# Kernel tuning notes

Measured on AMD Instinct MI355X. Metric: run time of the kernel, lower is better.

Reference implementation:

```python
import jax, jax.numpy as jnp
import numpy as np

B, CHAR_LEN, LSTM, VOCAB, NATTN = 4096, 64, 400, 73, 10

def _lstm_cell(x, h, c, W_ih, W_hh, b):
    # gates: [B, 4*LSTM] in (i, f, g, o) order, matching torch.nn.LSTMCell
    g = x @ W_ih.T + h @ W_hh.T + b
    i, f, gg, o = jnp.split(g, 4, axis=1)
    i = jax.nn.sigmoid(i); f = jax.nn.sigmoid(f)
    gg = jnp.tanh(gg); o = jax.nn.sigmoid(o)
    c_new = f * c + i * gg
    h_new = o * jnp.tanh(c_new)
    return h_new, c_new

def setup_inputs() -> dict:
    key = jax.random.key(0)
    ks = jax.random.split(key, 24)
    d = {}
    d['inputs'] = jax.random.normal(ks[0], (B, 3), jnp.float32)
    for n, k in zip(['h1','c1','h2','c2','h3','c3'], ks[1:7]):
        d[n] = jax.random.normal(k, (B, LSTM), jnp.float32) * 0.1
    d['kappa'] = jax.random.uniform(ks[7], (B, NATTN), jnp.float32) * 5.0
    d['w_prev'] = jax.random.uniform(ks[8], (B, VOCAB), jnp.float32)
    d['attention_values'] = jax.random.uniform(ks[9], (B, CHAR_LEN, VOCAB), jnp.float32)
    d['attention_lengths'] = jax.random.randint(ks[10], (B,), 1, CHAR_LEN + 1, jnp.int32)
    s = 0.05
    in1 = VOCAB + 3              # lstm1 input: [w, inputs]
    in23 = 3 + LSTM + VOCAB      # lstm2/3 input: [inputs, h, w]
    attn_in = VOCAB + 3 + LSTM
    d['W_ih1'] = jax.random.normal(ks[11], (4 * LSTM, in1), jnp.float32) * s
    d['W_hh1'] = jax.random.normal(ks[12], (4 * LSTM, LSTM), jnp.float32) * s
    d['b1'] = jax.random.normal(ks[13], (4 * LSTM,), jnp.float32) * s
    d['W_attn'] = jax.random.normal(ks[14], (3 * NATTN, attn_in), jnp.float32) * s
    d['b_attn'] = jax.random.normal(ks[15], (3 * NATTN,), jnp.float32) * s
    d['W_ih2'] = jax.random.normal(ks[16], (4 * LSTM, in23), jnp.float32) * s
    d['W_hh2'] = jax.random.normal(ks[17], (4 * LSTM, LSTM), jnp.float32) * s
    d['b2'] = jax.random.normal(ks[18], (4 * LSTM,), jnp.float32) * s
    d['W_ih3'] = jax.random.normal(ks[19], (4 * LSTM, in23), jnp.float32) * s
    d['W_hh3'] = jax.random.normal(ks[20], (4 * LSTM, LSTM), jnp.float32) * s
    d['b3'] = jax.random.normal(ks[21], (4 * LSTM,), jnp.float32) * s
    return d

def reference(inputs, h1, c1, h2, c2, h3, c3, kappa, w_prev, attention_values,
              attention_lengths, W_ih1, W_hh1, b1, W_attn, b_attn,
              W_ih2, W_hh2, b2, W_ih3, W_hh3, b3):
    char_len = attention_values.shape[1]
    # --- LSTM 1 ---
    s1_in = jnp.concatenate([w_prev, inputs], axis=1)
    h1n, c1n = _lstm_cell(s1_in, h1, c1, W_ih1, W_hh1, b1)
    # --- Gaussian-mixture location attention ---
    attn_in = jnp.concatenate([w_prev, inputs, h1n], axis=1)
    attn_params = jax.nn.softplus(attn_in @ W_attn.T + b_attn)
    alpha, beta, kap = jnp.split(attn_params, 3, axis=1)
    kap = kappa + kap / 25.0
    beta = jnp.maximum(beta, 0.01)
    u = jnp.arange(char_len, dtype=jnp.float32)[None, None, :]           # [1,1,C]
    phi = jnp.sum(alpha[:, :, None] *
                  jnp.exp(-jnp.square(kap[:, :, None] - u) / beta[:, :, None]),
                  axis=1)                                                 # [B,C]
    seq_mask = (jnp.arange(char_len)[None, :] < attention_lengths[:, None]).astype(jnp.float32)
    w = jnp.einsum('bc,bcv->bv', phi * seq_mask, attention_values)        # [B,V]
    # --- LSTM 2 & 3 ---
    s2_in = jnp.concatenate([inputs, h1n, w], axis=1)
    h2n, c2n = _lstm_cell(s2_in, h2, c2, W_ih2, W_hh2, b2)
    s3_in = jnp.concatenate([inputs, h2n, w], axis=1)
    h3n, c3n = _lstm_cell(s3_in, h3, c3, W_ih3, W_hh3, b3)
    return h3n
```

## Files before the change

kernel.cpp:

```cpp
#include <hip/hip_runtime.h>
#include <hip/hip_bf16.h>


#define B_SZ     4096
#define LSTM_N   400
#define NG       1600
#define VOCAB    73
#define NATTN    10
#define CHARLEN  64
#define KP1      512
#define KP23     896

typedef _Float16 half8 __attribute__((ext_vector_type(8)));
typedef __attribute__((ext_vector_type(4))) float floatx4;

__device__ __forceinline__ void gload_lds16(const void* g, void* l) {
    __builtin_amdgcn_global_load_lds(
        (const __attribute__((address_space(1))) void*)g,
        (__attribute__((address_space(3))) void*)l, 16, 0, 0);
}

__device__ __forceinline__ int lds_off(int r, int g) {
    return (r << 6) + ((((g ^ r) & 7)) << 3);
}

#define CW1   102400
#define CW23  179200
#define CWA   4096
#define CX1   262144
#define CXA   57344
#define CX23  253952
#define O1    (CW1)
#define O2    (O1 + CW23)
#define O3    (O2 + CW23)
#define O4    (O3 + CWA)
#define O5    (O4 + CX1)
#define O6    (O5 + CXA)
#define O7    (O6 + CX23)

__global__ __launch_bounds__(256) void pack_all(const float* __restrict__ Wih1,
                                                const float* __restrict__ Whh1,
                                                const float* __restrict__ Wih2,
                                                const float* __restrict__ Whh2,
                                                const float* __restrict__ Wih3,
                                                const float* __restrict__ Whh3,
                                                const float* __restrict__ W_attn,
                                                const float* __restrict__ w_prev,
                                                const float* __restrict__ inputs,
                                                const float* __restrict__ h1,
                                                const float* __restrict__ h2,
                                                const float* __restrict__ h3,
                                                _Float16* __restrict__ W1,
                                                _Float16* __restrict__ W2,
                                                _Float16* __restrict__ W3,
                                                _Float16* __restrict__ Wa,
                                                _Float16* __restrict__ X1,
                                                _Float16* __restrict__ XA,
                                                _Float16* __restrict__ X2,
                                                _Float16* __restrict__ X3)
{
    const int id = blockIdx.x * 256 + threadIdx.x;
    half8 hv;

    if (id < O1) {
        const int row = id >> 6;
        const int k0  = (id & 63) << 3;
        const int u = row >> 2, g = row & 3;
        const int src = g * 400 + u;
#pragma unroll
        for (int e = 0; e < 8; e++) {
            const int k = k0 + e;
            float x = 0.f;
            if (k < 76)           x = Wih1[(size_t)src * 76 + k];
            else if (k < 476)     x = Whh1[(size_t)src * 400 + (k - 76)];
            hv[e] = (_Float16)x;
        }
        *(half8*)(W1 + (size_t)row * KP1 + k0) = hv;
    } else if (id < O3) {
        const int id2 = id - O1;
        const bool is3 = (id2 >= CW23);
        const int id3 = is3 ? id2 - CW23 : id2;
        const int row = id3 / 112;
        const int k0  = (id3 - row * 112) << 3;
        const int u = row >> 2, g = row & 3;
        const int src = g * 400 + u;
        const float* Wih = is3 ? Wih3 : Wih2;
        const float* Whh = is3 ? Whh3 : Whh2;
#pragma unroll
        for (int e = 0; e < 8; e++) {
            const int k = k0 + e;
            float x = 0.f;
            if (k < 400)          x = Wih[(size_t)src * 476 + 3 + k];
            else if (k < 403)     x = Wih[(size_t)src * 476 + (k - 400)];
            else if (k < 476)     x = Wih[(size_t)src * 476 + k];
            else if (k < 876)     x = Whh[(size_t)src * 400 + (k - 476)];
            hv[e] = (_Float16)x;
        }
        *(half8*)((is3 ? W3 : W2) + (size_t)row * KP23 + k0) = hv;
    } else if (id < O4) {
        const int id4 = id - O3;
        const int row = id4 >> 6;
        const int k0  = (id4 & 63) << 3;
#pragma unroll
        for (int e = 0; e < 8; e++) {
            const int k = k0 + e;
            float x = 0.f;
            if (row < 30) {
                if (k < 400)      x = W_attn[(size_t)row * 476 + 76 + k];
                else if (k < 473) x = W_attn[(size_t)row * 476 + (k - 400)];
                else if (k < 476) x = W_attn[(size_t)row * 476 + 73 + (k - 473)];
            }
            hv[e] = (_Float16)x;
        }
        *(half8*)(Wa + (size_t)row * KP1 + k0) = hv;
    } else if (id < O5) {
        const int id5 = id - O4;
        const int b  = id5 >> 6;
        const int k0 = (id5 & 63) << 3;
#pragma unroll
        for (int e = 0; e < 8; e++) {
            const int k = k0 + e;
            float x = 0.f;
            if (k < 73)           x = w_prev[(size_t)b * 73 + k];
            else if (k < 76)      x = inputs[(size_t)b * 3 + (k - 73)];
            else if (k < 476)     x = h1[(size_t)b * 400 + (k - 76)];
            hv[e] = (_Float16)x;
        }
        *(half8*)(X1 + (size_t)b * KP1 + k0) = hv;
    } else if (id < O6) {
        const int id6 = id - O5;
        const int b  = id6 / 14;
        const int k0 = 400 + ((id6 - b * 14) << 3);
#pragma unroll
        for (int e = 0; e < 8; e++) {
            const int k = k0 + e;
            float x = 0.f;
            if (k < 473)          x = w_prev[(size_t)b * 73 + (k - 400)];
            else if (k < 476)     x = inputs[(size_t)b * 3 + (k - 473)];
            hv[e] = (_Float16)x;
        }
        *(half8*)(XA + (size_t)b * KP1 + k0) = hv;
    } else if (id < O7) {
        const int id7 = id - O6;
        const int b  = id7 / 62;
        const int k0 = 400 + ((id7 - b * 62) << 3);
        half8 h2v, h3v;
#pragma unroll
        for (int e = 0; e < 8; e++) {
            const int k = k0 + e;
            float x2 = 0.f, x3 = 0.f;
            if (k < 403)                    { x2 = inputs[(size_t)b * 3 + (k - 400)]; x3 = x2; }
            else if (k >= 476 && k < 876)   { x2 = h2[(size_t)b * 400 + (k - 476)];
                                              x3 = h3[(size_t)b * 400 + (k - 476)]; }
            h2v[e] = (_Float16)x2;
            h3v[e] = (_Float16)x3;
        }
        *(half8*)(X2 + (size_t)b * KP23 + k0) = h2v;
        *(half8*)(X3 + (size_t)b * KP23 + k0) = h3v;
    }
}

template<int KP>
__global__ __launch_bounds__(256) void gemm_fused_t(const _Float16* __restrict__ Wm,
                                                    const _Float16* __restrict__ X,
                                                    const float* __restrict__ bias,
                                                    const float* __restrict__ c_in,
                                                    _Float16* __restrict__ d1, int ld1,
                                                    _Float16* __restrict__ d2, int ld2,
                                                    float* __restrict__ fout)
{
    __shared__ _Float16 lds[3][192 * 64];

    const int t    = threadIdx.x;
    const int w    = t >> 6;
    const int lane = t & 63;
    const int quad = lane >> 4;
    const int l16  = lane & 15;
    const int fid  = blockIdx.y * 32 + blockIdx.x;
    const int xcd  = fid & 7;
    const int loc  = fid >> 3;
    const int bx   = xcd * 4 + loc / 25;
    const int by   = loc % 25;
    const int m0   = by * 64;
    const int n0   = bx * 128;
    const int wm   = (w >> 1) * 32;
    const int wn   = (w & 1) * 64;
    const int lr   = lane >> 3;
    const int gq   = (lane & 7) ^ lr;

    floatx4 acc[2][4] = {};

    auto stage = [&](int sb, int k0) {
#pragma unroll
        for (int s = 0; s < 2; s++)
            gload_lds16(Wm + (size_t)(m0 + w * 16 + s * 8 + lr) * KP + k0 + gq * 8,
                        &lds[sb][(w * 16 + s * 8) * 64]);
#pragma unroll
        for (int s = 0; s < 4; s++)
            gload_lds16(X + (size_t)(n0 + w * 32 + s * 8 + lr) * KP + k0 + gq * 8,
                        &lds[sb][(64 + w * 32 + s * 8) * 64]);
    };

    stage(0, 0);
    stage(1, 64);
    constexpr int NT = KP / 64;
#pragma unroll
    for (int kt = 0; kt < NT; kt++) {
        const int sb = kt % 3;
        if (kt + 2 < NT) {
            stage((kt + 2) % 3, (kt + 2) * 64);
            asm volatile("s_waitcnt vmcnt(12)" ::: "memory");
        } else if (kt + 1 < NT) {
            asm volatile("s_waitcnt vmcnt(6)" ::: "memory");
        } else {
            asm volatile("s_waitcnt vmcnt(0)" ::: "memory");
        }
        __builtin_amdgcn_s_barrier();
        __builtin_amdgcn_sched_barrier(0);

#pragma unroll
        for (int h = 0; h < 2; h++) {
            half8 af[2], bf[4];
#pragma unroll
            for (int i = 0; i < 2; i++)
                af[i] = *(const half8*)(&lds[sb][lds_off(wm + i * 16 + l16, h * 4 + quad)]);
#pragma unroll
            for (int i = 0; i < 4; i++)
                bf[i] = *(const half8*)(&lds[sb][lds_off(64 + wn + i * 16 + l16, h * 4 + quad)]);
            __builtin_amdgcn_s_setprio(1);
#pragma unroll
            for (int mt = 0; mt < 2; mt++)
#pragma unroll
                for (int nt = 0; nt < 4; nt++)
                    acc[mt][nt] = __builtin_amdgcn_mfma_f32_16x16x32_f16(
                        af[mt], bf[nt], acc[mt][nt], 0, 0, 0);
            __builtin_amdgcn_s_setprio(0);
        }
        __builtin_amdgcn_s_barrier();
    }
    __builtin_amdgcn_sched_barrier(0);

    const int u0 = m0 >> 2;
    float*    Cs   = (float*)&lds[0][0];
    _Float16* Hs16 = (_Float16*)&lds[1][0];
    float*    Hs32 = (float*)&lds[1][0];
    {
        const int bl = t >> 1;
        const int j0 = (t & 1) * 2;
#pragma unroll
        for (int j = 0; j < 2; j++) {
            floatx4 cv = *(const floatx4*)(c_in + (size_t)(n0 + bl) * LSTM_N
                                           + u0 + (j0 + j) * 4);
            *(floatx4*)(Cs + bl * 20 + (j0 + j) * 4) = cv;
        }
    }
    __syncthreads();

#pragma unroll
    for (int mt = 0; mt < 2; mt++) {
        const int ul = (wm >> 2) + mt * 4 + quad;
        const int u  = u0 + ul;
        const float bi  = bias[u];
        const float bff = bias[400 + u];
        const float bg  = bias[800 + u];
        const float bo  = bias[1200 + u];
#pragma unroll
        for (int nt = 0; nt < 4; nt++) {
            const int bl = wn + nt * 16 + l16;
            float gi = acc[mt][nt][0] + bi;
            float gf = acc[mt][nt][1] + bff;
            float gg = acc[mt][nt][2] + bg;
            float go = acc[mt][nt][3] + bo;
            float si = 1.f / (1.f + expf(-gi));
            float sf = 1.f / (1.f + expf(-gf));
            float so = 1.f / (1.f + expf(-go));
            float cn = sf * Cs[bl * 20 + ul] + si * tanhf(gg);
            float h  = so * tanhf(cn);
            if (fout) Hs32[bl * 20 + ul] = h;
            else      Hs16[bl * 24 + ul] = (_Float16)h;
        }
    }
    __syncthreads();

    if (fout) {
        const int bl = t >> 1;
        const int p0 = (t & 1) * 2;
#pragma unroll
        for (int j = 0; j < 2; j++) {
            floatx4 hvv = *(const floatx4*)(Hs32 + bl * 20 + (p0 + j) * 4);
            *(floatx4*)(fout + (size_t)(n0 + bl) * LSTM_N + u0 + (p0 + j) * 4) = hvv;
        }
    } else {
        const int bl = t >> 1;
        const int p  = t & 1;
        half8 hvv = *(const half8*)(Hs16 + bl * 24 + p * 8);
        *(half8*)(d1 + (size_t)(n0 + bl) * ld1 + u0 + p * 8) = hvv;
        if (d2) *(half8*)(d2 + (size_t)(n0 + bl) * ld2 + u0 + p * 8) = hvv;
    }
}

__global__ __launch_bounds__(256) void attn_fused(const _Float16* __restrict__ Wa,
                                                  const _Float16* __restrict__ XA,
                                                  const float* __restrict__ b_attn,
                                                  const float* __restrict__ kappa,
                                                  const float* __restrict__ AV,
                                                  const int* __restrict__ alen,
                                                  _Float16* __restrict__ X2,
                                                  _Float16* __restrict__ X3)
{
    __shared__ _Float16 Wa_s[30 * KP1];
    __shared__ float prm[4][32];
    __shared__ float phi_s[4][CHARLEN];

    const int t = threadIdx.x;
#pragma unroll
    for (int i = 0; i < 8; i++) {
        const int idx = t + i * 256;
        if (idx < 1920) {
            const int row = idx >> 6;
            const int c8  = (idx & 63) << 3;
            *(half8*)(&Wa_s[row * KP1 + c8]) = *(const half8*)(Wa + (size_t)row * KP1 + c8);
        }
    }
    __syncthreads();

    const int wave = t >> 6;
    const int lane = t & 63;
    const int b = blockIdx.x * 4 + wave;

    half8 xa = *(const half8*)(XA + (size_t)b * KP1 + lane * 8);
    float xf[8];
#pragma unroll
    for (int e = 0; e < 8; e++) xf[e] = (float)xa[e];

    float myp = 0.f;
#pragma unroll
    for (int m = 0; m < 30; m++) {
        half8 wv = *(const half8*)(&Wa_s[m * KP1 + lane * 8]);
        float s = 0.f;
#pragma unroll
        for (int e = 0; e < 8; e++) s += (float)wv[e] * xf[e];
#pragma unroll
        for (int sh = 32; sh >= 1; sh >>= 1) s += __shfl_xor(s, sh, 64);
        if (lane == m) myp = s;
    }

    if (lane < 30) {
        float p  = myp + b_attn[lane];
        float sp = (p > 20.f) ? p : log1pf(expf(p));
        float v;
        if (lane < 10)      v = sp;
        else if (lane < 20) v = fmaxf(sp, 0.01f);
        else                v = kappa[(size_t)b * NATTN + (lane - 20)] + sp * (1.f / 25.f);
        prm[wave][lane] = v;
    }
    __syncthreads();

    const int len = alen[b];
    {
        int c = lane;
        float phi = 0.f;
#pragma unroll
        for (int j = 0; j < NATTN; j++) {
            float d = prm[wave][20 + j] - (float)c;
            phi += prm[wave][j] * expf(-d * d / prm[wave][10 + j]);
        }
        phi_s[wave][c] = (c < len) ? phi : 0.f;
    }
    __syncthreads();

    for (int v0 = 0; v0 < VOCAB; v0 += 64) {
        const int v = v0 + lane;
        if (v < VOCAB) {
            const float* avb = AV + (size_t)b * CHARLEN * VOCAB + v;
            float s = 0.f;
            for (int c = 0; c < len; c++)
                s += phi_s[wave][c] * avb[(size_t)c * VOCAB];
            _Float16 wv = (_Float16)s;
            X2[(size_t)b * KP23 + 403 + v] = wv;
            X3[(size_t)b * KP23 + 403 + v] = wv;
        }
    }
}

extern "C" void kernel_launch(void* const* d_in, const int* in_sizes, int n_in,
                              void* d_out, int out_size, void* d_ws, size_t ws_size,
                              hipStream_t stream)
{
    const float* inputs = (const float*)d_in[0];
    const float* h1     = (const float*)d_in[1];
    const float* c1     = (const float*)d_in[2];
    const float* h2     = (const float*)d_in[3];
    const float* c2     = (const float*)d_in[4];
    const float* h3     = (const float*)d_in[5];
    const float* c3     = (const float*)d_in[6];
    const float* kappa  = (const float*)d_in[7];
    const float* w_prev = (const float*)d_in[8];
    const float* AV     = (const float*)d_in[9];
    const int*   alen   = (const int*)d_in[10];
    const float* W_ih1  = (const float*)d_in[11];
    const float* W_hh1  = (const float*)d_in[12];
    const float* b1     = (const float*)d_in[13];
    const float* W_attn = (const float*)d_in[14];
    const float* b_attn = (const float*)d_in[15];
    const float* W_ih2  = (const float*)d_in[16];
    const float* W_hh2  = (const float*)d_in[17];
    const float* b2     = (const float*)d_in[18];
    const float* W_ih3  = (const float*)d_in[19];
    const float* W_hh3  = (const float*)d_in[20];
    const float* b3     = (const float*)d_in[21];
    float* out = (float*)d_out;

    char* p = (char*)d_ws;
    _Float16* X1 = (_Float16*)p; p += (size_t)B_SZ * KP1 * 2;
    _Float16* XA = (_Float16*)p; p += (size_t)B_SZ * KP1 * 2;
    _Float16* X2 = (_Float16*)p; p += (size_t)B_SZ * KP23 * 2;
    _Float16* X3 = (_Float16*)p; p += (size_t)B_SZ * KP23 * 2;
    _Float16* W1 = (_Float16*)p; p += (size_t)NG * KP1 * 2;
    _Float16* W2 = (_Float16*)p; p += (size_t)NG * KP23 * 2;
    _Float16* W3 = (_Float16*)p; p += (size_t)NG * KP23 * 2;
    _Float16* Wa = (_Float16*)p; p += (size_t)64 * KP1 * 2;

    pack_all<<<O7 / 256, 256, 0, stream>>>(W_ih1, W_hh1, W_ih2, W_hh2,
                                           W_ih3, W_hh3, W_attn,
                                           w_prev, inputs, h1, h2, h3,
                                           W1, W2, W3, Wa, X1, XA, X2, X3);

    const dim3 fgrid(32, 25);

    gemm_fused_t<KP1><<<fgrid, 256, 0, stream>>>(W1, X1, b1, c1,
                                                 XA, KP1, X2, KP23, nullptr);
    attn_fused<<<B_SZ / 4, 256, 0, stream>>>(Wa, XA, b_attn, kappa, AV, alen, X2, X3);
    gemm_fused_t<KP23><<<fgrid, 256, 0, stream>>>(W2, X2, b2, c2,
                                                  X3, KP23, nullptr, 0, nullptr);
    gemm_fused_t<KP23><<<fgrid, 256, 0, stream>>>(W3, X3, b3, c3,
                                                  nullptr, 0, nullptr, 0, out);
}
```

Before: 289.7 us.

## Fuse pack, three LSTM GEMMs and attention into one persistent kernel with grid barriers

Replaces five separate kernel launches with a single persistent kernel of 512 blocks that runs the pack, LSTM1 GEMM, attention, LSTM2 and LSTM3 phases in order. Phases are separated by software grid barriers built on atomics. GEMM tiles are assigned per XCD so each XCD keeps a contiguous set of tiles. The aim is to remove launch gaps and tail effects between stages. In exchange it depends on all 512 blocks being co-resident, since the barrier spin has only a timeout escape, and it adds a memset launch and barrier overhead.

```diff
diff --git a/kernel.cpp b/kernel.cpp
--- a/kernel.cpp
+++ b/kernel.cpp
@@ -10,6 +10,8 @@
 #define CHARLEN  64
 #define KP1      512
 #define KP23     896
+#define NBLK     512
+#define NJOBS_A  1024
 
 typedef _Float16 half8 __attribute__((ext_vector_type(8)));
 typedef __attribute__((ext_vector_type(4))) float floatx4;
@@ -22,6 +24,28 @@
 
 __device__ __forceinline__ int lds_off(int r, int g) {
     return (r << 6) + ((((g ^ r) & 7)) << 3);
+}
+
+__device__ __forceinline__ void grid_barrier(int* bar, int phase, int nblk) {
+    __syncthreads();
+    if (threadIdx.x == 0) {
+        int* cnt = bar + phase * 64;
+        int* flg = cnt + 32;
+        int prev = __hip_atomic_fetch_add(cnt, 1, __ATOMIC_ACQ_REL,
+                                          __HIP_MEMORY_SCOPE_AGENT);
+        if (prev == nblk - 1) {
+            __hip_atomic_store(flg, 1, __ATOMIC_RELEASE,
+                               __HIP_MEMORY_SCOPE_AGENT);
+        } else {
+            int spins = 0;
+            while (__hip_atomic_load(flg, __ATOMIC_ACQUIRE,
+                                     __HIP_MEMORY_SCOPE_AGENT) == 0) {
+                __builtin_amdgcn_s_sleep(8);
+                if (++spins > 3000000) break;
+            }
+        }
+    }
+    __syncthreads();
 }
 
 #define CW1   102400
@@ -37,31 +61,22 @@
 #define O5    (O4 + CX1)
 #define O6    (O5 + CXA)
 #define O7    (O6 + CX23)
-
-__global__ __launch_bounds__(256) void pack_all(const float* __restrict__ Wih1,
-                                                const float* __restrict__ Whh1,
-                                                const float* __restrict__ Wih2,
-                                                const float* __restrict__ Whh2,
-                                                const float* __restrict__ Wih3,
-                                                const float* __restrict__ Whh3,
-                                                const float* __restrict__ W_attn,
-                                                const float* __restrict__ w_prev,
-                                                const float* __restrict__ inputs,
-                                                const float* __restrict__ h1,
-                                                const float* __restrict__ h2,
-                                                const float* __restrict__ h3,
-                                                _Float16* __restrict__ W1,
-                                                _Float16* __restrict__ W2,
-                                                _Float16* __restrict__ W3,
-                                                _Float16* __restrict__ Wa,
-                                                _Float16* __restrict__ X1,
-                                                _Float16* __restrict__ XA,
-                                                _Float16* __restrict__ X2,
-                                                _Float16* __restrict__ X3)
-{
-    const int id = blockIdx.x * 256 + threadIdx.x;
+#define NCHUNK (O7 / 256)
+
+__device__ __forceinline__ void pack_chunk(int id,
+    const float* __restrict__ Wih1, const float* __restrict__ Whh1,
+    const float* __restrict__ Wih2, const float* __restrict__ Whh2,
+    const float* __restrict__ Wih3, const float* __restrict__ Whh3,
+    const float* __restrict__ W_attn,
+    const float* __restrict__ w_prev, const float* __restrict__ inputs,
+    const float* __restrict__ h1, const float* __restrict__ h2,
+    const float* __restrict__ h3,
+    _Float16* __restrict__ W1, _Float16* __restrict__ W2,
+    _Float16* __restrict__ W3, _Float16* __restrict__ Wa,
+    _Float16* __restrict__ X1, _Float16* __restrict__ XA,
+    _Float16* __restrict__ X2, _Float16* __restrict__ X3)
+{
     half8 hv;
-
     if (id < O1) {
         const int row = id >> 6;
         const int k0  = (id & 63) << 3;
@@ -140,7 +155,7 @@
             hv[e] = (_Float16)x;
         }
         *(half8*)(XA + (size_t)b * KP1 + k0) = hv;
-    } else if (id < O7) {
+    } else {
         const int id7 = id - O6;
         const int b  = id7 / 62;
         const int k0 = 400 + ((id7 - b * 62) << 3);
@@ -161,26 +176,19 @@
 }
 
 template<int KP>
-__global__ __launch_bounds__(256) void gemm_fused_t(const _Float16* __restrict__ Wm,
-                                                    const _Float16* __restrict__ X,
-                                                    const float* __restrict__ bias,
-                                                    const float* __restrict__ c_in,
-                                                    _Float16* __restrict__ d1, int ld1,
-                                                    _Float16* __restrict__ d2, int ld2,
-                                                    float* __restrict__ fout)
-{
-    __shared__ _Float16 lds[3][192 * 64];
-
+__device__ __forceinline__ void gemm_job(int job, _Float16 (*lds)[192 * 64],
+    const _Float16* __restrict__ Wm, const _Float16* __restrict__ X,
+    const float* __restrict__ bias, const float* __restrict__ c_in,
+    _Float16* __restrict__ d1, int ld1,
+    _Float16* __restrict__ d2, int ld2, float* __restrict__ fout)
+{
     const int t    = threadIdx.x;
     const int w    = t >> 6;
     const int lane = t & 63;
     const int quad = lane >> 4;
     const int l16  = lane & 15;
-    const int fid  = blockIdx.y * 32 + blockIdx.x;
-    const int xcd  = fid & 7;
-    const int loc  = fid >> 3;
-    const int bx   = xcd * 4 + loc / 25;
-    const int by   = loc % 25;
+    const int by   = job % 25;
+    const int bx   = job / 25;
     const int m0   = by * 64;
     const int n0   = bx * 128;
     const int wm   = (w >> 1) * 32;
@@ -297,20 +305,31 @@
         *(half8*)(d1 + (size_t)(n0 + bl) * ld1 + u0 + p * 8) = hvv;
         if (d2) *(half8*)(d2 + (size_t)(n0 + bl) * ld2 + u0 + p * 8) = hvv;
     }
-}
-
-__global__ __launch_bounds__(256) void attn_fused(const _Float16* __restrict__ Wa,
-                                                  const _Float16* __restrict__ XA,
-                                                  const float* __restrict__ b_attn,
-                                                  const float* __restrict__ kappa,
-                                                  const float* __restrict__ AV,
-                                                  const int* __restrict__ alen,
-                                                  _Float16* __restrict__ X2,
-                                                  _Float16* __restrict__ X3)
-{
-    __shared__ _Float16 Wa_s[30 * KP1];
-    __shared__ float prm[4][32];
-    __shared__ float phi_s[4][CHARLEN];
+    __syncthreads();
+}
+
+template<int KP>
+__device__ __forceinline__ void gemm_phase(int bid, _Float16 (*lds)[192 * 64],
+    const _Float16* __restrict__ Wm, const _Float16* __restrict__ X,
+    const float* __restrict__ bias, const float* __restrict__ c_in,
+    _Float16* __restrict__ d1, int ld1,
+    _Float16* __restrict__ d2, int ld2, float* __restrict__ fout)
+{
+    const int xcd = bid & 7;
+    const int wi  = bid >> 3;
+    for (int j = wi; j < 100; j += 64)
+        gemm_job<KP>(xcd * 100 + j, lds, Wm, X, bias, c_in, d1, ld1, d2, ld2, fout);
+}
+
+__device__ __forceinline__ void attn_job(int job, _Float16* smem,
+    const _Float16* __restrict__ Wa, const _Float16* __restrict__ XA,
+    const float* __restrict__ b_attn, const float* __restrict__ kappa,
+    const float* __restrict__ AV, const int* __restrict__ alen,
+    _Float16* __restrict__ X2, _Float16* __restrict__ X3)
+{
+    _Float16* Wa_s = smem;
+    float* prm   = (float*)(smem + 30 * KP1);
+    float* phi_s = prm + 128;
 
     const int t = threadIdx.x;
 #pragma unroll
@@ -326,7 +345,7 @@
 
     const int wave = t >> 6;
     const int lane = t & 63;
-    const int b = blockIdx.x * 4 + wave;
+    const int b = job * 4 + wave;
 
     half8 xa = *(const half8*)(XA + (size_t)b * KP1 + lane * 8);
     float xf[8];
@@ -352,7 +371,7 @@
         if (lane < 10)      v = sp;
         else if (lane < 20) v = fmaxf(sp, 0.01f);
         else                v = kappa[(size_t)b * NATTN + (lane - 20)] + sp * (1.f / 25.f);
-        prm[wave][lane] = v;
+        prm[wave * 32 + lane] = v;
     }
     __syncthreads();
 
@@ -362,10 +381,10 @@
         float phi = 0.f;
 #pragma unroll
         for (int j = 0; j < NATTN; j++) {
-            float d = prm[wave][20 + j] - (float)c;
-            phi += prm[wave][j] * expf(-d * d / prm[wave][10 + j]);
-        }
-        phi_s[wave][c] = (c < len) ? phi : 0.f;
+            float d = prm[wave * 32 + 20 + j] - (float)c;
+            phi += prm[wave * 32 + j] * expf(-d * d / prm[wave * 32 + 10 + j]);
+        }
+        phi_s[wave * 64 + c] = (c < len) ? phi : 0.f;
     }
     __syncthreads();
 
@@ -375,12 +394,48 @@
             const float* avb = AV + (size_t)b * CHARLEN * VOCAB + v;
             float s = 0.f;
             for (int c = 0; c < len; c++)
-                s += phi_s[wave][c] * avb[(size_t)c * VOCAB];
+                s += phi_s[wave * 64 + c] * avb[(size_t)c * VOCAB];
             _Float16 wv = (_Float16)s;
             X2[(size_t)b * KP23 + 403 + v] = wv;
             X3[(size_t)b * KP23 + 403 + v] = wv;
         }
     }
+    __syncthreads();
+}
+
+__global__ __launch_bounds__(256, 2) void mega(
+    const float* Wih1, const float* Whh1, const float* Wih2, const float* Whh2,
+    const float* Wih3, const float* Whh3, const float* W_attn,
+    const float* w_prev, const float* inputs,
+    const float* h1, const float* h2, const float* h3,
+    const float* c1, const float* c2, const float* c3,
+    const float* b1, const float* b_attn, const float* b2, const float* b3,
+    const float* kappa, const float* AV, const int* alen,
+    _Float16* W1, _Float16* W2, _Float16* W3, _Float16* Wa,
+    _Float16* X1, _Float16* XA, _Float16* X2, _Float16* X3,
+    float* out, int* bar)
+{
+    __shared__ _Float16 lds[3][192 * 64];
+
+    const int bid = blockIdx.x;
+
+    for (int c = bid; c < NCHUNK; c += NBLK)
+        pack_chunk(c * 256 + threadIdx.x, Wih1, Whh1, Wih2, Whh2, Wih3, Whh3,
+                   W_attn, w_prev, inputs, h1, h2, h3,
+                   W1, W2, W3, Wa, X1, XA, X2, X3);
+    grid_barrier(bar, 0, NBLK);
+
+    gemm_phase<KP1>(bid, lds, W1, X1, b1, c1, XA, KP1, X2, KP23, nullptr);
+    grid_barrier(bar, 1, NBLK);
+
+    for (int job = bid; job < NJOBS_A; job += NBLK)
+        attn_job(job, &lds[0][0], Wa, XA, b_attn, kappa, AV, alen, X2, X3);
+    grid_barrier(bar, 2, NBLK);
+
+    gemm_phase<KP23>(bid, lds, W2, X2, b2, c2, X3, KP23, nullptr, 0, nullptr);
+    grid_barrier(bar, 3, NBLK);
+
+    gemm_phase<KP23>(bid, lds, W3, X3, b3, c3, nullptr, 0, nullptr, 0, out);
 }
 
 extern "C" void kernel_launch(void* const* d_in, const int* in_sizes, int n_in,
@@ -420,19 +475,13 @@
     _Float16* W2 = (_Float16*)p; p += (size_t)NG * KP23 * 2;
     _Float16* W3 = (_Float16*)p; p += (size_t)NG * KP23 * 2;
     _Float16* Wa = (_Float16*)p; p += (size_t)64 * KP1 * 2;
-
-    pack_all<<<O7 / 256, 256, 0, stream>>>(W_ih1, W_hh1, W_ih2, W_hh2,
-                                           W_ih3, W_hh3, W_attn,
-                                           w_prev, inputs, h1, h2, h3,
-                                           W1, W2, W3, Wa, X1, XA, X2, X3);
-
-    const dim3 fgrid(32, 25);
-
-    gemm_fused_t<KP1><<<fgrid, 256, 0, stream>>>(W1, X1, b1, c1,
-                                                 XA, KP1, X2, KP23, nullptr);
-    attn_fused<<<B_SZ / 4, 256, 0, stream>>>(Wa, XA, b_attn, kappa, AV, alen, X2, X3);
-    gemm_fused_t<KP23><<<fgrid, 256, 0, stream>>>(W2, X2, b2, c2,
-                                                  X3, KP23, nullptr, 0, nullptr);
-    gemm_fused_t<KP23><<<fgrid, 256, 0, stream>>>(W3, X3, b3, c3,
-                                                  nullptr, 0, nullptr, 0, out);
-}
+    int* bar = (int*)p;
+
+    hipMemsetAsync(bar, 0, 1024, stream);
+    mega<<<NBLK, 256, 0, stream>>>(W_ih1, W_hh1, W_ih2, W_hh2, W_ih3, W_hh3,
+                                   W_attn, w_prev, inputs, h1, h2, h3,
+                                   c1, c2, c3, b1, b_attn, b2, b3,
+                                   kappa, AV, alen,
+                                   W1, W2, W3, Wa, X1, XA, X2, X3,
+                                   out, bar);
+}
```

Result: slower. 610.5 us (+110.8%).
